# Optimization experiments

Measured on AMD Instinct MI355X. Metric: run time of the kernel, lower is better.

## Reference

```python
import jax, jax.numpy as jnp
import numpy as np

B, S, E, H = 4, 2048, 1024, 16
D = E // H  # head_dim = 64


def setup_inputs() -> dict:
    key = jax.random.key(0)
    ks = jax.random.split(key, 5)
    return {
        "hidden_states": jax.random.normal(ks[0], (B, S, E), dtype=jnp.float32),
        "c_attn_w": jax.random.normal(ks[1], (E, 3 * E), dtype=jnp.float32) * 0.02,
        "c_attn_b": jax.random.normal(ks[2], (3 * E,), dtype=jnp.float32) * 0.02,
        "c_proj_w": jax.random.normal(ks[3], (E, E), dtype=jnp.float32) * 0.02,
        "c_proj_b": jax.random.normal(ks[4], (E,), dtype=jnp.float32) * 0.02,
    }


def reference(hidden_states, c_attn_w, c_attn_b, c_proj_w, c_proj_b):
    b, s, e = hidden_states.shape
    # Conv1D c_attn: y = x @ W + b  -> qkv [b, s, 3E]
    qkv = hidden_states @ c_attn_w + c_attn_b
    q, k, v = jnp.split(qkv, 3, axis=-1)
    # split heads -> [b, H, s, D]
    def split_heads(t):
        return t.reshape(b, s, H, D).transpose(0, 2, 1, 3)
    q, k, v = split_heads(q), split_heads(k), split_heads(v)
    # QK^T scaled by sqrt(head_dim)
    scores = jnp.einsum("bhqd,bhkd->bhqk", q, k) / jnp.sqrt(
        jnp.asarray(D, dtype=q.dtype)
    )
    # causal mask (tril), masked positions get dtype min
    causal = jnp.tril(jnp.ones((s, s), dtype=bool))[None, None]
    mask_value = jnp.finfo(scores.dtype).min
    scores = jnp.where(causal, scores, mask_value)
    attn = jax.nn.softmax(scores, axis=-1)
    # attend to values, merge heads
    out = jnp.einsum("bhqk,bhkd->bhqd", attn, v)
    out = out.transpose(0, 2, 1, 3).reshape(b, s, e)
    # Conv1D c_proj
    return out @ c_proj_w + c_proj_b
```

## Files before the change

kernel.cpp:

```cpp
#include <hip/hip_runtime.h>
#include <hip/hip_bf16.h>
#include <cstdint>
#include <cstddef>

#define BB 4
#define SS 2048
#define EE 1024
#define HH 16
#define DD 64

typedef __attribute__((ext_vector_type(8))) short bf16x8;
typedef __attribute__((ext_vector_type(4))) float f32x4;

__device__ __forceinline__ short f2bf(float f) {
    union { float f; uint32_t u; } x; x.f = f;
    uint32_t r = (x.u + 0x7fffu + ((x.u >> 16) & 1u)) >> 16;
    return (short)r;
}
__device__ __forceinline__ short f2bf_fast(float f) {
    union { float f; uint32_t u; } x; x.f = f;
    return (short)((x.u + 0x8000u) >> 16);
}

__device__ __forceinline__ void gload16(const void* g, void* l) {
    __builtin_amdgcn_global_load_lds(
        (__attribute__((address_space(1))) uint32_t*)(uintptr_t)g,
        (__attribute__((address_space(3))) uint32_t*)(uint32_t)(uintptr_t)l,
        16, 0, 0);
}

#define WAIT_BARRIER(N)                                          \
    asm volatile("s_waitcnt vmcnt(" #N ")" ::: "memory");        \
    __builtin_amdgcn_s_barrier();                                \
    __builtin_amdgcn_sched_barrier(0);

template<int CTRL>
__device__ __forceinline__ float dppmove(float v) {
    return __int_as_float(__builtin_amdgcn_update_dpp(
        0, __float_as_int(v), CTRL, 0xf, 0xf, true));
}
#define ROW_REDUCE(vals, OP)                                             \
    _Pragma("unroll") for (int _r = 0; _r < 4; ++_r) {                   \
        vals[_r] = OP(vals[_r], dppmove<0xB1>(vals[_r]));                \
        vals[_r] = OP(vals[_r], dppmove<0x4E>(vals[_r]));                \
        vals[_r] = OP(vals[_r], dppmove<0x124>(vals[_r]));               \
        vals[_r] = OP(vals[_r], dppmove<0x128>(vals[_r]));               \
    }
__device__ __forceinline__ float opmax(float a, float b) { return fmaxf(a, b); }
__device__ __forceinline__ float opsum(float a, float b) { return a + b; }

__global__ void prep_kernel(const float* __restrict__ hs, short* __restrict__ Xb,
                            const float* __restrict__ attn_w, short* __restrict__ WqkvT,
                            const float* __restrict__ proj_w, short* __restrict__ WprojT)
{
    __shared__ float ts[32][33];
    int bid = blockIdx.x;
    const int t = threadIdx.x;
    if (bid < 2048) {
        const int n4 = (BB * SS * EE) / 4;
        const int stride = 2048 * 256;
        for (int i = bid * 256 + t; i < n4; i += stride) {
            float4 v = reinterpret_cast<const float4*>(hs)[i];
            short4 o;
            o.x = f2bf(v.x); o.y = f2bf(v.y); o.z = f2bf(v.z); o.w = f2bf(v.w);
            reinterpret_cast<short4*>(Xb)[i] = o;
        }
        return;
    }
    bid -= 2048;
    const float* in; short* out; int ncols, bx, by;
    if (bid < 3072) { in = attn_w; out = WqkvT; ncols = 3 * EE; bx = bid % 96; by = bid / 96; }
    else { bid -= 3072; in = proj_w; out = WprojT; ncols = EE; bx = bid % 32; by = bid / 32; }
    const int r = t >> 3, c4 = (t & 7) * 4;
    const int n0 = bx * 32, k0 = by * 32;
    float4 v = *reinterpret_cast<const float4*>(&in[(size_t)(k0 + r) * ncols + n0 + c4]);
    ts[c4 + 0][r] = v.x; ts[c4 + 1][r] = v.y; ts[c4 + 2][r] = v.z; ts[c4 + 3][r] = v.w;
    __syncthreads();
    short4 ov;
    ov.x = f2bf(ts[r][c4 + 0]); ov.y = f2bf(ts[r][c4 + 1]);
    ov.z = f2bf(ts[r][c4 + 2]); ov.w = f2bf(ts[r][c4 + 3]);
    *reinterpret_cast<short4*>(&out[(size_t)(n0 + r) * EE + k0 + c4]) = ov;
}

template<int MODE>
__global__ __launch_bounds__(256, 2)
void gemm128(const short* __restrict__ A, const short* __restrict__ Bt,
             const float* __restrict__ bias,
             short* __restrict__ Qo, short* __restrict__ Ko, short* __restrict__ Vo,
             float* __restrict__ Co)
{
    __shared__ short As[3][4096];
    __shared__ short Bs[3][4096];
    const int tid  = threadIdx.x;
    const int lane = tid & 63, wid = tid >> 6;
    const int wr = wid >> 1, wc = wid & 1;
    const int l15 = lane & 15, lhi = lane >> 4;
    const int m0 = blockIdx.y * 128, n0 = blockIdx.x * 128;
    const int sr   = lane >> 2;
    const int scol = 8 * ((lane & 3) ^ ((lane >> 3) & 3));
    const int rdx  = (lhi ^ ((l15 >> 1) & 3)) << 4;

    f32x4 acc[4][4] = {};

#define G_STAGE(tt, bufi)                                                        \
    {                                                                            \
        const int kk = (tt) * 32;                                                \
        _Pragma("unroll")                                                        \
        for (int p = 0; p < 2; ++p) {                                            \
            const int c = wid * 2 + p;                                           \
            gload16(&A [(size_t)(m0 + c * 16 + sr) * EE + kk + scol],            \
                    (char*)&As[bufi][0] + c * 1024);                             \
            gload16(&Bt[(size_t)(n0 + c * 16 + sr) * EE + kk + scol],            \
                    (char*)&Bs[bufi][0] + c * 1024);                             \
        }                                                                        \
    }

#define G_ITER(kt_, cb, sb, DOSTAGE, WAITCODE)                                   \
    {                                                                            \
        if (DOSTAGE) { G_STAGE((kt_) + 2, sb) }                                  \
        bf16x8 af[4], bfr[4];                                                    \
        _Pragma("unroll")                                                        \
        for (int mm = 0; mm < 4; ++mm)                                           \
            af[mm] = *reinterpret_cast<const bf16x8*>(                           \
                (const char*)&As[cb][0] + (wr * 64 + mm * 16 + l15) * 64 + rdx); \
        _Pragma("unroll")                                                        \
        for (int nn = 0; nn < 4; ++nn)                                           \
            bfr[nn] = *reinterpret_cast<const bf16x8*>(                          \
                (const char*)&Bs[cb][0] + (wc * 64 + nn * 16 + l15) * 64 + rdx); \
        _Pragma("unroll")                                                        \
        for (int mm = 0; mm < 4; ++mm)                                           \
            _Pragma("unroll")                                                    \
            for (int nn = 0; nn < 4; ++nn)                                       \
                acc[mm][nn] = __builtin_amdgcn_mfma_f32_16x16x32_bf16(           \
                    af[mm], bfr[nn], acc[mm][nn], 0, 0, 0);                      \
        WAITCODE                                                                 \
    }

    G_STAGE(0, 0)
    G_STAGE(1, 1)
    WAIT_BARRIER(4)

    for (int kb = 0; kb < 30; kb += 3) {
        G_ITER(kb + 0, 0, 2, true, WAIT_BARRIER(4))
        G_ITER(kb + 1, 1, 0, true, WAIT_BARRIER(4))
        G_ITER(kb + 2, 2, 1, true, WAIT_BARRIER(4))
    }
    G_ITER(30, 0, 2, false, WAIT_BARRIER(0))
    G_ITER(31, 1, 0, false, )
#undef G_ITER
#undef G_STAGE

    if (MODE == 0) {
        const int part = n0 >> 10;
        #pragma unroll
        for (int mm = 0; mm < 4; ++mm) {
            #pragma unroll
            for (int nn = 0; nn < 4; ++nn) {
                const int gcol = n0 + wc * 64 + nn * 16 + l15;
                const float bv = bias[gcol];
                const int e = gcol & 1023;
                const int h = e >> 6, d = e & 63;
                const int grow0 = m0 + wr * 64 + mm * 16 + lhi * 4;
                const int bidx = grow0 >> 11;
                const int s0 = grow0 & 2047;
                const int bh = bidx * HH + h;
                if (part == 2) {
                    short4 pk;
                    pk.x = f2bf(acc[mm][nn][0] + bv);
                    pk.y = f2bf(acc[mm][nn][1] + bv);
                    pk.z = f2bf(acc[mm][nn][2] + bv);
                    pk.w = f2bf(acc[mm][nn][3] + bv);
                    *reinterpret_cast<short4*>(&Vo[((size_t)bh * DD + d) * SS + s0]) = pk;
                } else if (part == 0) {
                    #pragma unroll
                    for (int r = 0; r < 4; ++r)
                        Qo[((size_t)bh * SS + s0 + r) * DD + d] = f2bf((acc[mm][nn][r] + bv) * 0.18033688f);
                } else {
                    #pragma unroll
                    for (int r = 0; r < 4; ++r)
                        Ko[((size_t)bh * SS + s0 + r) * DD + d] = f2bf(acc[mm][nn][r] + bv);
                }
            }
        }
    } else {
        #pragma unroll
        for (int mm = 0; mm < 4; ++mm) {
            #pragma unroll
            for (int nn = 0; nn < 4; ++nn) {
                const int gcol = n0 + wc * 64 + nn * 16 + l15;
                const float bv = bias[gcol];
                #pragma unroll
                for (int r = 0; r < 4; ++r) {
                    const int grow = m0 + wr * 64 + mm * 16 + lhi * 4 + r;
                    Co[(size_t)grow * EE + gcol] = acc[mm][nn][r] + bv;
                }
            }
        }
    }
}

__global__ __launch_bounds__(512, 2)
void attn_kernel(const short* __restrict__ Q, const short* __restrict__ K,
                 const short* __restrict__ Vt, short* __restrict__ CTX)
{
    __shared__ short Ks[4][4096];
    __shared__ short Vs[4][4096];
    __shared__ short Ps[8][1024];
    const int tid  = threadIdx.x;
    const int lane = tid & 63, wid = tid >> 6;
    const int l15 = lane & 15, lhi = lane >> 4;
    const int bid  = blockIdx.x;
    const int bh   = (bid & 7) * 8 + ((bid >> 3) & 7);
    const int pair = bid >> 6;
    const int b = bh >> 4, h = bh & 15;
    const size_t base = (size_t)bh * (SS * DD);
    const short* VtBase = Vt + (size_t)bh * (DD * SS);
    char* const pw = (char*)&Ps[wid][0];

    const int srow = lane >> 3;
    const int scol = 8 * ((lane & 7) ^ srow);

#define ATT_STAGE(tt, bufi)                                                          \
    {                                                                                \
        const int kk = (tt) * 64;                                                    \
        gload16(&K[base + (size_t)(kk + wid * 8 + srow) * DD + scol],                \
                (char*)&Ks[bufi][0] + wid * 1024);                                   \
        gload16(&VtBase[(size_t)(wid * 8 + srow) * SS + kk + scol],                  \
                (char*)&Vs[bufi][0] + wid * 1024);                                   \
    }

    for (int phase = 0; phase < 2; ++phase) {
        const int t = phase ? (15 - pair) : pair;
        const int q0 = t * 128;
        const int qbase = q0 + wid * 16;
        const int nkt = 2 * t + 2;

        bf16x8 qa[2];
        qa[0] = *reinterpret_cast<const bf16x8*>(&Q[base + (size_t)(qbase + l15) * DD + lhi * 8]);
        qa[1] = *reinterpret_cast<const bf16x8*>(&Q[base + (size_t)(qbase + l15) * DD + 32 + lhi * 8]);

        f32x4 o[4] = {};
        float psum[4] = {0.f, 0.f, 0.f, 0.f};

        ATT_STAGE(0, 0)
        ATT_STAGE(1, 1)
        WAIT_BARRIER(2)

        for (int kt = 0; kt < nkt; ++kt) {
            const int cur = kt & 3;
            const int k0 = kt * 64;
            const bool active = (k0 <= qbase + 15);

            if (kt + 2 < nkt) { ATT_STAGE(kt + 2, (kt + 2) & 3) }

            f32x4 sc[4];
            if (active) {
                __builtin_amdgcn_s_setprio(1);
                #pragma unroll
                for (int n = 0; n < 4; ++n) {
                    const int row = n * 16 + l15;
                    f32x4 cacc = {};
                    #pragma unroll
                    for (int ks = 0; ks < 2; ++ks) {
                        const int byteoff = (ks * 64 + lhi * 16) ^ ((l15 & 7) << 4);
                        bf16x8 kb = *reinterpret_cast<const bf16x8*>((const char*)&Ks[cur][0] + row * 128 + byteoff);
                        cacc = __builtin_amdgcn_mfma_f32_16x16x32_bf16(qa[ks], kb, cacc, 0, 0, 0);
                    }
                    sc[n] = cacc;
                }
                __builtin_amdgcn_s_setprio(0);

                if (k0 + 63 > qbase) {
                    #pragma unroll
                    for (int n = 0; n < 4; ++n) {
                        const int col = k0 + n * 16 + l15;
                        #pragma unroll
                        for (int r = 0; r < 4; ++r) {
                            const int qrow = qbase + lhi * 4 + r;
                            if (col > qrow) sc[n][r] = -1e30f;
                        }
                    }
                }
                #pragma unroll
                for (int n = 0; n < 4; ++n)
                    #pragma unroll
                    for (int r = 0; r < 4; ++r) sc[n][r] = __builtin_amdgcn_exp2f(sc[n][r]);
                #pragma unroll
                for (int r = 0; r < 4; ++r)
                    psum[r] += (sc[0][r] + sc[1][r]) + (sc[2][r] + sc[3][r]);
                #pragma unroll
                for (int n = 0; n < 4; ++n)
                    #pragma unroll
                    for (int r = 0; r < 4; ++r) {
                        const int q = lhi * 4 + r;
                        const int cb = (n * 32 + l15 * 2) ^ ((q & 7) << 4);
                        *reinterpret_cast<short*>(pw + q * 128 + cb) = f2bf_fast(sc[n][r]);
                    }
                bf16x8 pa[2];
                #pragma unroll
                for (int ks = 0; ks < 2; ++ks)
                    pa[ks] = *reinterpret_cast<const bf16x8*>(
                        pw + l15 * 128 + ((ks * 64 + lhi * 16) ^ ((l15 & 7) << 4)));
                __builtin_amdgcn_s_setprio(1);
                #pragma unroll
                for (int dg = 0; dg < 4; ++dg) {
                    const int row = dg * 16 + l15;
                    #pragma unroll
                    for (int ks = 0; ks < 2; ++ks) {
                        const int byteoff = (ks * 64 + lhi * 16) ^ ((l15 & 7) << 4);
                        bf16x8 vb = *reinterpret_cast<const bf16x8*>((const char*)&Vs[cur][0] + row * 128 + byteoff);
                        o[dg] = __builtin_amdgcn_mfma_f32_16x16x32_bf16(pa[ks], vb, o[dg], 0, 0, 0);
                    }
                }
                __builtin_amdgcn_s_setprio(0);
            }

            if (kt < nkt - 2)       { WAIT_BARRIER(2) }
            else if (kt == nkt - 2) { WAIT_BARRIER(0) }
        }
        __syncthreads();

        float lrow[4];
        #pragma unroll
        for (int r = 0; r < 4; ++r) lrow[r] = psum[r];
        ROW_REDUCE(lrow, opsum)

        #pragma unroll
        for (int dg = 0; dg < 4; ++dg)
            #pragma unroll
            for (int r = 0; r < 4; ++r) {
                int s = qbase + lhi * 4 + r;
                float val = o[dg][r] / lrow[r];
                CTX[(size_t)(b * SS + s) * EE + h * DD + dg * 16 + l15] = f2bf(val);
            }
    }
#undef ATT_STAGE
}

extern "C" void kernel_launch(void* const* d_in, const int* in_sizes, int n_in,
                              void* d_out, int out_size, void* d_ws, size_t ws_size,
                              hipStream_t stream) {
    const float* hs     = (const float*)d_in[0];
    const float* attn_w = (const float*)d_in[1];
    const float* attn_b = (const float*)d_in[2];
    const float* proj_w = (const float*)d_in[3];
    const float* proj_b = (const float*)d_in[4];
    float* out = (float*)d_out;

    char* ws = (char*)d_ws;
    short* Xb    = (short*)(ws + 0);
    short* WqkvT = (short*)(ws + 16777216);
    short* WprojT= (short*)(ws + 23068672);
    short* Qb    = (short*)(ws + 25165824);
    short* Kb    = (short*)(ws + 41943040);
    short* Vb    = (short*)(ws + 58720256);
    short* CTX   = Xb;

    prep_kernel<<<dim3(2048 + 3072 + 1024), dim3(256), 0, stream>>>(
        hs, Xb, attn_w, WqkvT, proj_w, WprojT);

    gemm128<0><<<dim3(3 * EE / 128, BB * SS / 128), dim3(256), 0, stream>>>(
        Xb, WqkvT, attn_b, Qb, Kb, Vb, nullptr);

    attn_kernel<<<dim3(512), dim3(512), 0, stream>>>(Qb, Kb, Vb, CTX);

    gemm128<1><<<dim3(EE / 128, BB * SS / 128), dim3(256), 0, stream>>>(
        CTX, WprojT, proj_b, nullptr, nullptr, nullptr, out);
}
```

Before: 159.8 us.

## Switch GEMM to BK=64 double buffering with a new LDS swizzle

The 128x128 GEMM moves from a three-stage pipeline with K-tile 32 to a two-stage double buffer with K-tile 64. Each stage covers two MFMA k-substeps, and the LDS layout now uses 128-byte rows with an XOR swizzle over 8 chunks. This halves the number of barriers and loop iterations. In exchange, the prefetch depth drops to one tile ahead and each barrier waits for all outstanding loads (vmcnt 0), so global-load latency may be less well hidden.

Result: no change. 162.0 us (+1.3%).

```diff
diff --git a/kernel.cpp b/kernel.cpp
--- a/kernel.cpp
+++ b/kernel.cpp
@@ -89,64 +89,66 @@
              short* __restrict__ Qo, short* __restrict__ Ko, short* __restrict__ Vo,
              float* __restrict__ Co)
 {
-    __shared__ short As[3][4096];
-    __shared__ short Bs[3][4096];
+    __shared__ short As[2][8192];
+    __shared__ short Bs[2][8192];
     const int tid  = threadIdx.x;
     const int lane = tid & 63, wid = tid >> 6;
     const int wr = wid >> 1, wc = wid & 1;
     const int l15 = lane & 15, lhi = lane >> 4;
     const int m0 = blockIdx.y * 128, n0 = blockIdx.x * 128;
-    const int sr   = lane >> 2;
-    const int scol = 8 * ((lane & 3) ^ ((lane >> 3) & 3));
-    const int rdx  = (lhi ^ ((l15 >> 1) & 3)) << 4;
+    const int srow = lane >> 3;
+    const int scol = 8 * ((lane & 7) ^ srow);
 
     f32x4 acc[4][4] = {};
 
 #define G_STAGE(tt, bufi)                                                        \
     {                                                                            \
-        const int kk = (tt) * 32;                                                \
+        const int kk = (tt) * 64;                                                \
         _Pragma("unroll")                                                        \
-        for (int p = 0; p < 2; ++p) {                                            \
-            const int c = wid * 2 + p;                                           \
-            gload16(&A [(size_t)(m0 + c * 16 + sr) * EE + kk + scol],            \
+        for (int p = 0; p < 4; ++p) {                                            \
+            const int c = wid * 4 + p;                                           \
+            gload16(&A [(size_t)(m0 + c * 8 + srow) * EE + kk + scol],           \
                     (char*)&As[bufi][0] + c * 1024);                             \
-            gload16(&Bt[(size_t)(n0 + c * 16 + sr) * EE + kk + scol],            \
+            gload16(&Bt[(size_t)(n0 + c * 8 + srow) * EE + kk + scol],           \
                     (char*)&Bs[bufi][0] + c * 1024);                             \
         }                                                                        \
     }
 
-#define G_ITER(kt_, cb, sb, DOSTAGE, WAITCODE)                                   \
+#define G_ITER(kt_, cb, DOSTAGE, DOBAR)                                          \
     {                                                                            \
-        if (DOSTAGE) { G_STAGE((kt_) + 2, sb) }                                  \
-        bf16x8 af[4], bfr[4];                                                    \
+        if (DOSTAGE) { G_STAGE((kt_) + 1, (cb) ^ 1) }                            \
         _Pragma("unroll")                                                        \
-        for (int mm = 0; mm < 4; ++mm)                                           \
-            af[mm] = *reinterpret_cast<const bf16x8*>(                           \
-                (const char*)&As[cb][0] + (wr * 64 + mm * 16 + l15) * 64 + rdx); \
-        _Pragma("unroll")                                                        \
-        for (int nn = 0; nn < 4; ++nn)                                           \
-            bfr[nn] = *reinterpret_cast<const bf16x8*>(                          \
-                (const char*)&Bs[cb][0] + (wc * 64 + nn * 16 + l15) * 64 + rdx); \
-        _Pragma("unroll")                                                        \
-        for (int mm = 0; mm < 4; ++mm)                                           \
+        for (int ks = 0; ks < 2; ++ks) {                                         \
+            bf16x8 af[4], bfr[4];                                                \
+            _Pragma("unroll")                                                    \
+            for (int mm = 0; mm < 4; ++mm)                                       \
+                af[mm] = *reinterpret_cast<const bf16x8*>(                       \
+                    (const char*)&As[cb][0] + (wr * 64 + mm * 16 + l15) * 128    \
+                    + ((ks * 64 + lhi * 16) ^ ((l15 & 7) << 4)));                \
             _Pragma("unroll")                                                    \
             for (int nn = 0; nn < 4; ++nn)                                       \
-                acc[mm][nn] = __builtin_amdgcn_mfma_f32_16x16x32_bf16(           \
-                    af[mm], bfr[nn], acc[mm][nn], 0, 0, 0);                      \
-        WAITCODE                                                                 \
+                bfr[nn] = *reinterpret_cast<const bf16x8*>(                      \
+                    (const char*)&Bs[cb][0] + (wc * 64 + nn * 16 + l15) * 128    \
+                    + ((ks * 64 + lhi * 16) ^ ((l15 & 7) << 4)));                \
+            _Pragma("unroll")                                                    \
+            for (int mm = 0; mm < 4; ++mm)                                       \
+                _Pragma("unroll")                                                \
+                for (int nn = 0; nn < 4; ++nn)                                   \
+                    acc[mm][nn] = __builtin_amdgcn_mfma_f32_16x16x32_bf16(       \
+                        af[mm], bfr[nn], acc[mm][nn], 0, 0, 0);                  \
+        }                                                                        \
+        if (DOBAR) { WAIT_BARRIER(0) }                                           \
     }
 
     G_STAGE(0, 0)
-    G_STAGE(1, 1)
-    WAIT_BARRIER(4)
-
-    for (int kb = 0; kb < 30; kb += 3) {
-        G_ITER(kb + 0, 0, 2, true, WAIT_BARRIER(4))
-        G_ITER(kb + 1, 1, 0, true, WAIT_BARRIER(4))
-        G_ITER(kb + 2, 2, 1, true, WAIT_BARRIER(4))
-    }
-    G_ITER(30, 0, 2, false, WAIT_BARRIER(0))
-    G_ITER(31, 1, 0, false, )
+    WAIT_BARRIER(0)
+
+    for (int kb = 0; kb < 14; kb += 2) {
+        G_ITER(kb + 0, 0, true, true)
+        G_ITER(kb + 1, 1, true, true)
+    }
+    G_ITER(14, 0, true, true)
+    G_ITER(15, 1, false, false)
 #undef G_ITER
 #undef G_STAGE
 
```
